# Optimization experiments

Hardware: AMD Instinct MI355X
Metric: run time of the kernel (lower is better)

The kernel has to match this reference:

```python
import jax, jax.numpy as jnp
import numpy as np
from functools import partial

MIN_PERSISTENCE = 0.0
BIG = jnp.float32(1e30)


def pairwise_dist(points):
    # points: [n, d] -> [n, n] Euclidean distances (Vietoris-Rips filtration values on edges)
    sq = jnp.sum(points * points, axis=-1)
    d2 = sq[:, None] + sq[None, :] - 2.0 * (points @ points.T)
    return jnp.sqrt(jnp.clip(d2, 0.0))


def h0_persistence(points):
    """0-dim persistent homology of the Vietoris-Rips filtration.

    H0 bars: every point is born at filtration 0; components merge at MST edge
    lengths (single-linkage). Deaths = the n-1 MST edge weights, in the order
    Prim's algorithm adds them (the boundary-matrix column reduction for dim 0
    yields exactly these pairs). One essential class (infinite bar) is dropped.
    """
    n = points.shape[0]
    dist = pairwise_dist(points)  # [n, n]

    in_tree = jnp.zeros((n,), dtype=bool).at[0].set(True)
    mind = dist[0]  # min distance from each node to the current tree

    def step(carry, _):
        mind, in_tree = carry
        masked = jnp.where(in_tree, BIG, mind)
        j = jnp.argmin(masked)          # next vertex merged into the tree
        death = masked[j]               # filtration value at which its component dies
        in_tree = in_tree.at[j].set(True)
        mind = jnp.minimum(mind, dist[j])
        return (mind, in_tree), death

    (_, _), deaths = jax.lax.scan(step, (mind, in_tree), None, length=n - 1)

    births = jnp.zeros_like(deaths)
    diagram = jnp.stack([births, deaths], axis=-1)  # [n-1, 2]
    # min_persistence threshold: zero out bars with persistence below threshold
    keep = (deaths - births) >= MIN_PERSISTENCE
    return jnp.where(keep[:, None], diagram, 0.0)


def setup_inputs() -> dict:
    key = jax.random.key(0)
    x = jax.random.normal(key, (8192, 64), dtype=jnp.float32)
    return {"x": x}


def reference(x):
    # PersistentHomologyLayer.forward with edge_index=None -> point-cloud VR persistence.
    return h0_persistence(x)
```

## Files before the change

### kernel.cpp

```cpp
#include <hip/hip_runtime.h>
#include <math.h>

#define N 8192
#define DIM 64
#define CAP_E 2000000
#define INLINE_V 8064

typedef unsigned long long u64;
typedef unsigned int u32;
typedef unsigned short u16;

__global__ void zero_out_kernel(float* __restrict__ out, int n) {
    int i = blockIdx.x * blockDim.x + threadIdx.x;
    if (i < n) out[i] = 0.0f;
}

__global__ __launch_bounds__(256) void norms_kernel(const float* __restrict__ x,
                                                    float* __restrict__ norms) {
    int i = blockIdx.x * blockDim.x + threadIdx.x;
    const float* row = x + (size_t)i * DIM;
    float acc = 0.f;
    #pragma unroll
    for (int k = 0; k < DIM; k++) { float v = row[k]; acc = __builtin_fmaf(v, v, acc); }
    norms[i] = acc;
}

__device__ inline void stage_tiles(const float* __restrict__ x, int bi, int bj, int t,
                                   float (*As)[65], float (*Bs)[65]) {
    int r = t >> 2, c0 = (t & 3) * 16;
    const float4* pa = (const float4*)(x + (size_t)(bi * 64 + r) * DIM + c0);
    const float4* pb = (const float4*)(x + (size_t)(bj * 64 + r) * DIM + c0);
    #pragma unroll
    for (int q = 0; q < 4; q++) {
        float4 a = pa[q], b = pb[q];
        int c = c0 + q * 4;
        As[c + 0][r] = a.x; As[c + 1][r] = a.y; As[c + 2][r] = a.z; As[c + 3][r] = a.w;
        Bs[c + 0][r] = b.x; Bs[c + 1][r] = b.y; Bs[c + 2][r] = b.z; Bs[c + 3][r] = b.w;
    }
}

__device__ inline void tile_d2(const float (*As)[65], const float (*Bs)[65],
                               const float ni[4], const float nj[4],
                               int tx, int ty, u32 d2b[4][4]) {
    float acc[4][4] = {};
    #pragma unroll 4
    for (int k = 0; k < 64; k++) {
        float av[4], bv[4];
        #pragma unroll
        for (int r = 0; r < 4; r++) av[r] = As[k][ty * 4 + r];
        #pragma unroll
        for (int c = 0; c < 4; c++) bv[c] = Bs[k][tx * 4 + c];
        #pragma unroll
        for (int r = 0; r < 4; r++)
            #pragma unroll
            for (int c = 0; c < 4; c++)
                acc[r][c] = __builtin_fmaf(av[r], bv[c], acc[r][c]);
    }
    #pragma unroll
    for (int r = 0; r < 4; r++)
        #pragma unroll
        for (int c = 0; c < 4; c++) {
            float d2 = __builtin_fmaf(-2.0f, acc[r][c], ni[r] + nj[c]);
            d2 = d2 < 0.f ? 0.f : d2;
            d2b[r][c] = __float_as_uint(d2);
        }
}

__global__ void init_kernel(u64* bestR, u64* bestC, u16* comp16, u32* deg, u32* ctr) {
    int i = blockIdx.x * blockDim.x + threadIdx.x;
    if (i < 8192) { bestR[i] = ~0ull; bestC[i] = ~0ull; comp16[i] = (u16)i; deg[i] = 0; }
    if (i < 8) ctr[i] = 0;
}

__global__ __launch_bounds__(256) void scan_fused(const float* __restrict__ x,
                                                  const float* __restrict__ norms,
                                                  const u16* __restrict__ comp16,
                                                  u64* __restrict__ bestR,
                                                  const u32* __restrict__ ctr) {
    if (ctr[1]) return;
    int bi = blockIdx.y, bj = blockIdx.x;
    if (bj < bi) return;
    __shared__ float As[64][65], Bs[64][65];
    __shared__ u16 rc[64], cc[64];
    __shared__ u64 rowBest[64], colBest[64];
    int t = threadIdx.x;
    stage_tiles(x, bi, bj, t, As, Bs);
    if (t < 64) {
        rc[t] = comp16[bi * 64 + t];
        cc[t] = comp16[bj * 64 + t];
        rowBest[t] = ~0ull; colBest[t] = ~0ull;
    }
    __syncthreads();
    int tx = t & 15, ty = t >> 4;
    float ni[4], nj[4];
    #pragma unroll
    for (int r = 0; r < 4; r++) ni[r] = norms[bi * 64 + ty * 4 + r];
    #pragma unroll
    for (int c = 0; c < 4; c++) nj[c] = norms[bj * 64 + tx * 4 + c];
    u32 d2b[4][4];
    tile_d2(As, Bs, ni, nj, tx, ty, d2b);

    #pragma unroll
    for (int r = 0; r < 4; r++) {
        u16 rcv = rc[ty * 4 + r];
        int gi = bi * 64 + ty * 4 + r;
        u64 best = ~0ull;
        #pragma unroll
        for (int c = 0; c < 4; c++) {
            if (cc[tx * 4 + c] != rcv) {
                int gj = bj * 64 + tx * 4 + c;
                u32 lo = gi < gj ? (u32)gi : (u32)gj;
                u32 hi = gi < gj ? (u32)gj : (u32)gi;
                u64 key = ((u64)d2b[r][c] << 26) | ((u64)lo << 13) | hi;
                if (key < best) best = key;
            }
        }
        if (best != ~0ull) atomicMin(&rowBest[ty * 4 + r], best);
    }
    #pragma unroll
    for (int c = 0; c < 4; c++) {
        u16 ccv = cc[tx * 4 + c];
        int gj = bj * 64 + tx * 4 + c;
        u64 best = ~0ull;
        #pragma unroll
        for (int r = 0; r < 4; r++) {
            if (rc[ty * 4 + r] != ccv) {
                int gi = bi * 64 + ty * 4 + r;
                u32 lo = gi < gj ? (u32)gi : (u32)gj;
                u32 hi = gi < gj ? (u32)gj : (u32)gi;
                u64 key = ((u64)d2b[r][c] << 26) | ((u64)lo << 13) | hi;
                if (key < best) best = key;
            }
        }
        if (best != ~0ull) atomicMin(&colBest[tx * 4 + c], best);
    }
    __syncthreads();
    if (t < 64) {
        if (rowBest[t] != ~0ull) atomicMin(&bestR[bi * 64 + t], rowBest[t]);
        if (colBest[t] != ~0ull) atomicMin(&bestR[bj * 64 + t], colBest[t]);
    }
}

__global__ void fold_kernel(u64* bestR, u64* bestC, const u16* comp16, const u32* ctr) {
    if (ctr[1]) return;
    int i = blockIdx.x * blockDim.x + threadIdx.x;
    if (i < 8192) {
        u64 k = bestR[i];
        if (k != ~0ull) { atomicMin(&bestC[comp16[i]], k); bestR[i] = ~0ull; }
    }
}

__global__ __launch_bounds__(1024) void merge_kernel(u16* comp16, u64* bestC,
                                                     u64* mstKeys, u32* ctr) {
    __shared__ u16 ping[8192], pong[8192];
    __shared__ unsigned char act[8192];
    __shared__ u32 cnt_s;
    if (ctr[1]) return;
    int t = threadIdx.x;
    if (t == 0) cnt_s = 0;
    for (int c = t; c < 8192; c += 1024) {
        u64 key = bestC[c];
        u16 par = (u16)c;
        if (key != ~0ull) {
            u32 a = (u32)(key >> 13) & 8191u, b = (u32)key & 8191u;
            u16 ca = comp16[a];
            u16 cv = (ca == (u16)c) ? comp16[b] : ca;
            u64 k2 = bestC[cv];
            bool mutual = false;
            if (k2 != ~0ull) {
                u32 a2 = (u32)(k2 >> 13) & 8191u, b2 = (u32)k2 & 8191u;
                u16 ca2 = comp16[a2];
                u16 cv2 = (ca2 == cv) ? comp16[b2] : ca2;
                mutual = (cv2 == (u16)c);
            }
            par = cv;
            if (mutual && (u32)c < (u32)cv) par = (u16)c;
            bool add = (!mutual) || ((u32)c < (u32)cv);
            if (add) {
                u32 idx = atomicAdd(&ctr[0], 1u);
                if (idx < 8192u) mstKeys[idx] = key;
            }
        }
        ping[c] = par;
        act[c] = 0;
    }
    __syncthreads();
    for (int c = t; c < 8192; c += 1024) bestC[c] = ~0ull;
    __syncthreads();
    for (int it = 0; it < 13; it++) {
        for (int c = t; c < 8192; c += 1024) pong[c] = ping[ping[c]];
        __syncthreads();
        for (int c = t; c < 8192; c += 1024) ping[c] = pong[c];
        __syncthreads();
    }
    for (int v = t; v < 8192; v += 1024) {
        u16 nc = ping[comp16[v]];
        comp16[v] = nc;
        act[nc] = 1;
    }
    __syncthreads();
    u32 local = 0;
    for (int c = t; c < 8192; c += 1024) local += act[c];
    atomicAdd(&cnt_s, local);
    __syncthreads();
    if (t == 0 && cnt_s == 1) ctr[1] = 1;
}

__global__ __launch_bounds__(1024) void sort_kernel(const u64* __restrict__ mstKeys,
                                                    u32* __restrict__ sortedWB,
                                                    const u32* __restrict__ ctr) {
    __shared__ u64 keys[8192];
    int t = threadIdx.x;
    u32 m = ctr[0]; if (m > 8191u) m = 8191u;
    for (int i = t; i < 8192; i += 1024) keys[i] = (i < (int)m) ? mstKeys[i] : ~0ull;
    __syncthreads();
    for (u32 k = 2; k <= 8192; k <<= 1)
        for (u32 j = k >> 1; j > 0; j >>= 1) {
            for (int i = t; i < 8192; i += 1024) {
                u32 ixj = (u32)i ^ j;
                if (ixj > (u32)i) {
                    u64 a = keys[i], b = keys[ixj];
                    bool up = ((i & k) == 0);
                    if ((a > b) == up) { keys[i] = b; keys[ixj] = a; }
                }
            }
            __syncthreads();
        }
    for (int i = t; i < 8192; i += 1024)
        sortedWB[i] = (i < 8191) ? (u32)(keys[i] >> 26) : 0xFFFFFFFFu;
}

__global__ __launch_bounds__(256) void collect_kernel(const float* __restrict__ x,
                                                      const float* __restrict__ norms,
                                                      const u32* __restrict__ sortedWB,
                                                      u64* __restrict__ edges,
                                                      u32* __restrict__ ctr) {
    __shared__ float As[64][65], Bs[64][65];
    __shared__ u32 sw[8191];
    int bi = blockIdx.y, bj = blockIdx.x;
    if (bj < bi) return;
    int t = threadIdx.x;
    stage_tiles(x, bi, bj, t, As, Bs);
    for (int i = t; i < 8191; i += 256) sw[i] = sortedWB[i];
    __syncthreads();
    u32 wmin = sw[0], wmax = sw[8190];
    int tx = t & 15, ty = t >> 4;
    float ni[4], nj[4];
    #pragma unroll
    for (int r = 0; r < 4; r++) ni[r] = norms[bi * 64 + ty * 4 + r];
    #pragma unroll
    for (int c = 0; c < 4; c++) nj[c] = norms[bj * 64 + tx * 4 + c];
    u32 d2b[4][4];
    tile_d2(As, Bs, ni, nj, tx, ty, d2b);

    #pragma unroll
    for (int r = 0; r < 4; r++) {
        int gi = bi * 64 + ty * 4 + r;
        #pragma unroll
        for (int c = 0; c < 4; c++) {
            int gj = bj * 64 + tx * 4 + c;
            if (gj <= gi) continue;
            u32 wb = d2b[r][c];
            if (wb < wmin || wb > wmax) continue;
            int lo = 0, hi = 8190;
            while (lo < hi) { int mid = (lo + hi) >> 1; if (sw[mid] < wb) lo = mid + 1; else hi = mid; }
            if (sw[lo] == wb) {
                u32 idx = atomicAdd(&ctr[3], 1u);
                if (idx < CAP_E)
                    edges[idx] = ((u64)(u32)lo << 26) | ((u64)(u32)gi << 13) | (u32)gj;
                else
                    atomicOr(&ctr[2], 16u);
            }
        }
    }
}

__global__ void degcnt_kernel(const u64* __restrict__ edges, u32* __restrict__ deg,
                              const u32* __restrict__ ctr) {
    u32 m = ctr[3]; if (m > CAP_E) m = CAP_E;
    for (u32 idx = blockIdx.x * 256u + threadIdx.x; idx < m; idx += gridDim.x * 256u) {
        u64 e = edges[idx];
        atomicAdd(&deg[(u32)(e >> 13) & 8191u], 1u);
        atomicAdd(&deg[(u32)e & 8191u], 1u);
    }
}

__global__ __launch_bounds__(1024) void offs_kernel(const u32* __restrict__ deg,
                                                    u32* __restrict__ offs,
                                                    u32* __restrict__ cur) {
    __shared__ u32 partial[1024];
    int t = threadIdx.x;
    u32 loc[8], s = 0;
    #pragma unroll
    for (int e = 0; e < 8; e++) { loc[e] = deg[t * 8 + e]; s += loc[e]; }
    partial[t] = s;
    __syncthreads();
    for (int d = 1; d < 1024; d <<= 1) {
        u32 v = (t >= d) ? partial[t - d] : 0;
        __syncthreads();
        partial[t] += v;
        __syncthreads();
    }
    u32 run = t ? partial[t - 1] : 0;
    #pragma unroll
    for (int e = 0; e < 8; e++) { offs[t * 8 + e] = run; cur[t * 8 + e] = run; run += loc[e]; }
    if (t == 1023) offs[8192] = run;
}

__global__ void fill_kernel(const u64* __restrict__ edges, u32* __restrict__ cur,
                            u32* __restrict__ adj, const u32* __restrict__ ctr) {
    u32 m = ctr[3]; if (m > CAP_E) m = CAP_E;
    for (u32 idx = blockIdx.x * 256u + threadIdx.x; idx < m; idx += gridDim.x * 256u) {
        u64 e = edges[idx];
        u32 rk = (u32)(e >> 26) & 8191u;
        u32 i = (u32)(e >> 13) & 8191u, j = (u32)e & 8191u;
        u32 p1 = atomicAdd(&cur[i], 1u); adj[p1] = (rk << 13) | j;
        u32 p2 = atomicAdd(&cur[j], 1u); adj[p2] = (rk << 13) | i;
    }
}

__global__ __launch_bounds__(256) void adj4_kernel(const u32* __restrict__ offs,
                                                   const u32* __restrict__ adjG,
                                                   uint4* __restrict__ adj4,
                                                   u64* __restrict__ ovf) {
    int v = blockIdx.x * 256 + threadIdx.x;
    if (v >= N) return;
    u32 o0 = offs[v], o1 = offs[v + 1], dg = o1 - o0;
    u32 e[4] = {0xFFFFFFFFu, 0xFFFFFFFFu, 0xFFFFFFFFu, 0xFFFFFFFFu};
    u32 nin = dg <= 4u ? dg : 3u;
    for (u32 q = 0; q < nin; q++) e[q] = adjG[o0 + q];
    if (dg > 4u) e[3] = 0xFFFFFFFEu;
    adj4[v] = make_uint4(e[0], e[1], e[2], e[3]);
    ovf[v] = ((u64)dg << 32) | o0;
}

__device__ __forceinline__ u32 dpp_min_u32(u32 x) {
    u32 y;
    y = (u32)__builtin_amdgcn_update_dpp((int)0xFFFFFFFF, (int)x, 0x111, 0xf, 0xf, false); x = y < x ? y : x;
    y = (u32)__builtin_amdgcn_update_dpp((int)0xFFFFFFFF, (int)x, 0x112, 0xf, 0xf, false); x = y < x ? y : x;
    y = (u32)__builtin_amdgcn_update_dpp((int)0xFFFFFFFF, (int)x, 0x114, 0xf, 0xf, false); x = y < x ? y : x;
    y = (u32)__builtin_amdgcn_update_dpp((int)0xFFFFFFFF, (int)x, 0x118, 0xf, 0xf, false); x = y < x ? y : x;
    y = (u32)__builtin_amdgcn_update_dpp((int)0xFFFFFFFF, (int)x, 0x142, 0xa, 0xf, false); x = y < x ? y : x;
    y = (u32)__builtin_amdgcn_update_dpp((int)0xFFFFFFFF, (int)x, 0x143, 0xc, 0xf, false); x = y < x ? y : x;
    return x;
}

__global__ __launch_bounds__(256) void gprim_kernel(const uint4* __restrict__ adj4,
                                                    const u64* __restrict__ ovf,
                                                    const u32* __restrict__ adjG,
                                                    u32* __restrict__ seqv,
                                                    u32* __restrict__ ctr) {
    __shared__ uint4 sAdj4[INLINE_V];
    __shared__ u32 sMind32[8192];
    const int t = threadIdx.x;
    for (int i = t; i < INLINE_V; i += 256) sAdj4[i] = adj4[i];
    for (int i = t; i < 8192; i += 256) sMind32[i] = 0x3FFFu;
    __syncthreads();
    if (t >= 64) return;
    __builtin_amdgcn_s_setprio(3);
    const int lane = t;
    if (lane == 0) sMind32[0] = 0xFFFFFFFFu;
    u64 ins0 = (lane == 0) ? 1ull : 0ull, ins1 = 0ull;
    u32 cmin = 0xFFFFFFFFu;
    u32 v = 0u, Lv = 0u;

#define PROC(e) do { \
        u32 _e = (e); \
        u32 _far = _e & 8191u; \
        u32 _slot = _far >> 6; \
        u64 _w = (_slot & 64u) ? ins1 : ins0; \
        bool _ok = (_e < 0x04000000u) && (((_far ^ (u32)lane) & 63u) == 0u) \
                   && (((_w >> (_slot & 63u)) & 1ull) == 0ull); \
        patch = (_ok && _e < patch) ? _e : patch; \
        if (_ok) atomicMin(&sMind32[((u32)lane << 7) + _slot], _e >> 13); \
    } while (0)

    for (int step = 0; step < N - 1; ++step) {
        uint2 rp = *(const uint2*)&sMind32[(Lv << 7) + 2u * (u32)lane];
        uint4 A = (v < (u32)INLINE_V) ? sAdj4[v] : adj4[v];
        u32 patch = 0xFFFFFFFFu;
        PROC(A.x); PROC(A.y); PROC(A.z);
        if (A.w == 0xFFFFFFFEu) {
            u64 od = ovf[v];
            u32 o0 = (u32)od, dgv = (u32)(od >> 32);
            u32 q = 3;
            for (; q + 4 <= dgv; q += 4) {
                u32 e0 = adjG[o0 + q], e1 = adjG[o0 + q + 1];
                u32 e2 = adjG[o0 + q + 2], e3 = adjG[o0 + q + 3];
                PROC(e0); PROC(e1); PROC(e2); PROC(e3);
            }
            for (; q < dgv; q++) { u32 e = adjG[o0 + q]; PROC(e); }
        } else {
            PROC(A.w);
        }
        cmin = patch < cmin ? patch : cmin;
        u32 m0 = rp.x, m1 = rp.y;
        u32 s0 = ((u32)lane << 1), s1 = s0 | 1u;
        u32 vslot = v >> 6;
        u32 k0 = (m0 < 0x3FFFu && s0 != vslot) ? ((m0 << 13) | (s0 << 6) | Lv) : 0xFFFFFFFFu;
        u32 k1 = (m1 < 0x3FFFu && s1 != vslot) ? ((m1 << 13) | (s1 << 6) | Lv) : 0xFFFFFFFFu;
        u32 rowMin = k0 < k1 ? k0 : k1;
        u32 R = dpp_min_u32(rowMin);
        u32 xc = ((u32)lane == Lv) ? patch : cmin;
        u32 C = dpp_min_u32(xc);
        u32 Rs = (u32)__builtin_amdgcn_readlane((int)R, 63);
        u32 Cs = (u32)__builtin_amdgcn_readlane((int)C, 63);
        u32 g = Rs < Cs ? Rs : Cs;
        if ((u32)lane == Lv) cmin = Rs < patch ? Rs : patch;
        if (g >= (0x3FFFu << 13)) { if (lane == 0) atomicOr(&ctr[2], 2u); break; }
        if (lane == 0) seqv[step] = g;
        v = g & 8191u; Lv = v & 63u;
        u32 nslot = v >> 6;
        bool mine = ((u32)lane == Lv);
        u64 bit = 1ull << (nslot & 63u);
        ins0 |= (mine && nslot < 64u) ? bit : 0ull;
        ins1 |= (mine && nslot >= 64u) ? bit : 0ull;
        if (mine) sMind32[(Lv << 7) + nslot] = 0xFFFFFFFFu;
    }
#undef PROC
}

__global__ void gather_kernel(const u32* __restrict__ seqv,
                              const u32* __restrict__ sortedWB,
                              float* __restrict__ out) {
    int s = blockIdx.x * blockDim.x + threadIdx.x;
    if (s < N - 1) {
        u32 p = seqv[s];
        u32 rk = p >> 13;
        out[2 * s + 1] = sqrtf(__uint_as_float(sortedWB[rk]));
    }
}

extern "C" void kernel_launch(void* const* d_in, const int* in_sizes, int n_in,
                              void* d_out, int out_size, void* d_ws, size_t ws_size,
                              hipStream_t stream) {
    const float* x = (const float*)d_in[0];
    float* out = (float*)d_out;

    char* ws = (char*)d_ws;
    size_t o = 0;
    u64* bestR    = (u64*)(ws + o); o += 8192 * 8;
    u64* bestC    = (u64*)(ws + o); o += 8192 * 8;
    u64* mstKeys  = (u64*)(ws + o); o += 8192 * 8;
    u64* edges    = (u64*)(ws + o); o += (size_t)CAP_E * 8;
    float* norms  = (float*)(ws + o); o += 8192 * 4;
    u32* sortedWB = (u32*)(ws + o); o += 8192 * 4;
    u32* deg      = (u32*)(ws + o); o += 8192 * 4;
    u32* offs     = (u32*)(ws + o); o += 8200 * 4;
    u32* cur      = (u32*)(ws + o); o += 8192 * 4;
    u32* seqv     = (u32*)(ws + o); o += 8192 * 4;
    u32* adj      = (u32*)(ws + o); o += (size_t)CAP_E * 2 * 4;
    uint4* adj4   = (uint4*)(ws + o); o += 8192 * 16;
    u64* ovf      = (u64*)(ws + o); o += 8192 * 8;
    u16* comp16   = (u16*)(ws + o); o += 8192 * 2;
    u32* ctr      = (u32*)(ws + o); o += 256;

    zero_out_kernel<<<(out_size + 255) / 256, 256, 0, stream>>>(out, out_size);
    norms_kernel<<<32, 256, 0, stream>>>(x, norms);
    init_kernel<<<32, 256, 0, stream>>>(bestR, bestC, comp16, deg, ctr);

    for (int r = 0; r < 13; r++) {
        scan_fused<<<dim3(128, 128), 256, 0, stream>>>(x, norms, comp16, bestR, ctr);
        fold_kernel<<<32, 256, 0, stream>>>(bestR, bestC, comp16, ctr);
        merge_kernel<<<1, 1024, 0, stream>>>(comp16, bestC, mstKeys, ctr);
    }

    sort_kernel<<<1, 1024, 0, stream>>>(mstKeys, sortedWB, ctr);
    collect_kernel<<<dim3(128, 128), 256, 0, stream>>>(x, norms, sortedWB, edges, ctr);
    degcnt_kernel<<<512, 256, 0, stream>>>(edges, deg, ctr);
    offs_kernel<<<1, 1024, 0, stream>>>(deg, offs, cur);
    fill_kernel<<<512, 256, 0, stream>>>(edges, cur, adj, ctr);
    adj4_kernel<<<32, 256, 0, stream>>>(offs, adj, adj4, ovf);
    gprim_kernel<<<1, 256, 0, stream>>>(adj4, ovf, adj, seqv, ctr);
    gather_kernel<<<32, 256, 0, stream>>>(seqv, sortedWB, out);
}
```

Measured before the change: 5.991 ms.

## Remove per-step global writes and branches from the serial Prim loop

The single-wavefront Prim loop no longer writes its step sequence to global memory on every step. Instead it stores a marker holding the step and rank in the shared mind array, and dumps that array once at the end. The gather kernel then scatters results by vertex. Other changes make the loop branch-free: atomicMin runs unconditionally with a sentinel value, the last-lane writes go to dummy slots, and the adjacency fetch always reads LDS. High-degree vertices now read their full list from the overflow path. The aim is to cut latency on the serial critical path, at the cost of some extra LDS atomics per step.

```diff
diff --git a/kernel.cpp b/kernel.cpp
--- a/kernel.cpp
+++ b/kernel.cpp
@@ -327,7 +327,7 @@
     if (v >= N) return;
     u32 o0 = offs[v], o1 = offs[v + 1], dg = o1 - o0;
     u32 e[4] = {0xFFFFFFFFu, 0xFFFFFFFFu, 0xFFFFFFFFu, 0xFFFFFFFFu};
-    u32 nin = dg <= 4u ? dg : 3u;
+    u32 nin = dg <= 4u ? dg : 0u;
     for (u32 q = 0; q < nin; q++) e[q] = adjG[o0 + q];
     if (dg > 4u) e[3] = 0xFFFFFFFEu;
     adj4[v] = make_uint4(e[0], e[1], e[2], e[3]);
@@ -348,13 +348,13 @@
 __global__ __launch_bounds__(256) void gprim_kernel(const uint4* __restrict__ adj4,
                                                     const u64* __restrict__ ovf,
                                                     const u32* __restrict__ adjG,
-                                                    u32* __restrict__ seqv,
+                                                    u32* __restrict__ seqm,
                                                     u32* __restrict__ ctr) {
     __shared__ uint4 sAdj4[INLINE_V];
-    __shared__ u32 sMind32[8192];
+    __shared__ u32 sMind32[8192 + 64];
     const int t = threadIdx.x;
     for (int i = t; i < INLINE_V; i += 256) sAdj4[i] = adj4[i];
-    for (int i = t; i < 8192; i += 256) sMind32[i] = 0x3FFFu;
+    for (int i = t; i < 8192 + 64; i += 256) sMind32[i] = 0x3FFFu;
     __syncthreads();
     if (t >= 64) return;
     __builtin_amdgcn_s_setprio(3);
@@ -363,6 +363,10 @@
     u64 ins0 = (lane == 0) ? 1ull : 0ull, ins1 = 0ull;
     u32 cmin = 0xFFFFFFFFu;
     u32 v = 0u, Lv = 0u;
+    const u32 baseLoc = (u32)lane << 7;
+    const u32 c0k = ((u32)lane * 2u) << 6;
+    const u32 c1k = c0k + 64u;
+    const u32 dummyLoc = 8192u + (u32)lane;
 
 #define PROC(e) do { \
         u32 _e = (e); \
@@ -372,33 +376,38 @@
         bool _ok = (_e < 0x04000000u) && (((_far ^ (u32)lane) & 63u) == 0u) \
                    && (((_w >> (_slot & 63u)) & 1ull) == 0ull); \
         patch = (_ok && _e < patch) ? _e : patch; \
-        if (_ok) atomicMin(&sMind32[((u32)lane << 7) + _slot], _e >> 13); \
+        u32 _val = _ok ? (_e >> 13) : 0xFFFFFFFFu; \
+        atomicMin(&sMind32[baseLoc + _slot], _val); \
     } while (0)
 
     for (int step = 0; step < N - 1; ++step) {
         uint2 rp = *(const uint2*)&sMind32[(Lv << 7) + 2u * (u32)lane];
-        uint4 A = (v < (u32)INLINE_V) ? sAdj4[v] : adj4[v];
+        uint4 A = sAdj4[v < (u32)INLINE_V ? v : 0u];
         u32 patch = 0xFFFFFFFFu;
-        PROC(A.x); PROC(A.y); PROC(A.z);
-        if (A.w == 0xFFFFFFFEu) {
+        if (__builtin_expect(v >= (u32)INLINE_V || A.w == 0xFFFFFFFEu, 0)) {
             u64 od = ovf[v];
             u32 o0 = (u32)od, dgv = (u32)(od >> 32);
-            u32 q = 3;
-            for (; q + 4 <= dgv; q += 4) {
-                u32 e0 = adjG[o0 + q], e1 = adjG[o0 + q + 1];
-                u32 e2 = adjG[o0 + q + 2], e3 = adjG[o0 + q + 3];
-                PROC(e0); PROC(e1); PROC(e2); PROC(e3);
-            }
-            for (; q < dgv; q++) { u32 e = adjG[o0 + q]; PROC(e); }
+            u32 iL = dgv ? dgv - 1u : 0u;
+            for (u32 q = 0; q < dgv; q += 4) {
+                u32 i1 = (q + 1u > iL) ? iL : q + 1u;
+                u32 i2 = (q + 2u > iL) ? iL : q + 2u;
+                u32 i3 = (q + 3u > iL) ? iL : q + 3u;
+                u32 e0 = adjG[o0 + q], e1 = adjG[o0 + i1];
+                u32 e2 = adjG[o0 + i2], e3 = adjG[o0 + i3];
+                PROC(e0);
+                if (q + 1u < dgv) PROC(e1);
+                if (q + 2u < dgv) PROC(e2);
+                if (q + 3u < dgv) PROC(e3);
+            }
         } else {
-            PROC(A.w);
+            PROC(A.x); PROC(A.y); PROC(A.z); PROC(A.w);
         }
         cmin = patch < cmin ? patch : cmin;
         u32 m0 = rp.x, m1 = rp.y;
         u32 s0 = ((u32)lane << 1), s1 = s0 | 1u;
         u32 vslot = v >> 6;
-        u32 k0 = (m0 < 0x3FFFu && s0 != vslot) ? ((m0 << 13) | (s0 << 6) | Lv) : 0xFFFFFFFFu;
-        u32 k1 = (m1 < 0x3FFFu && s1 != vslot) ? ((m1 << 13) | (s1 << 6) | Lv) : 0xFFFFFFFFu;
+        u32 k0 = (m0 < 0x3FFFu && s0 != vslot) ? ((m0 << 13) | c0k | Lv) : 0xFFFFFFFFu;
+        u32 k1 = (m1 < 0x3FFFu && s1 != vslot) ? ((m1 << 13) | c1k | Lv) : 0xFFFFFFFFu;
         u32 rowMin = k0 < k1 ? k0 : k1;
         u32 R = dpp_min_u32(rowMin);
         u32 xc = ((u32)lane == Lv) ? patch : cmin;
@@ -408,26 +417,36 @@
         u32 g = Rs < Cs ? Rs : Cs;
         if ((u32)lane == Lv) cmin = Rs < patch ? Rs : patch;
         if (g >= (0x3FFFu << 13)) { if (lane == 0) atomicOr(&ctr[2], 2u); break; }
-        if (lane == 0) seqv[step] = g;
         v = g & 8191u; Lv = v & 63u;
         u32 nslot = v >> 6;
         bool mine = ((u32)lane == Lv);
         u64 bit = 1ull << (nslot & 63u);
         ins0 |= (mine && nslot < 64u) ? bit : 0ull;
         ins1 |= (mine && nslot >= 64u) ? bit : 0ull;
-        if (mine) sMind32[(Lv << 7) + nslot] = 0xFFFFFFFFu;
+        u32 marker = 0x80000000u | ((u32)step << 13) | (g >> 13);
+        u32 wloc = mine ? ((Lv << 7) + nslot) : dummyLoc;
+        sMind32[wloc] = marker;
     }
 #undef PROC
-}
-
-__global__ void gather_kernel(const u32* __restrict__ seqv,
+
+    for (int it = 0; it < 32; ++it) {
+        int idx = it * 64 + lane;
+        uint4 m4 = *(const uint4*)&sMind32[idx * 4];
+        ((uint4*)seqm)[idx] = m4;
+    }
+}
+
+__global__ void gather_kernel(const u32* __restrict__ seqm,
                               const u32* __restrict__ sortedWB,
                               float* __restrict__ out) {
-    int s = blockIdx.x * blockDim.x + threadIdx.x;
-    if (s < N - 1) {
-        u32 p = seqv[s];
-        u32 rk = p >> 13;
-        out[2 * s + 1] = sqrtf(__uint_as_float(sortedWB[rk]));
+    int v = blockIdx.x * blockDim.x + threadIdx.x;
+    if (v < N) {
+        u32 m = seqm[v];
+        u32 stp = (m >> 13) & 8191u;
+        if ((m & 0x80000000u) && stp < 8191u) {
+            u32 rk = m & 8191u;
+            out[2 * stp + 1] = sqrtf(__uint_as_float(sortedWB[rk]));
+        }
     }
 }
 
@@ -448,7 +467,7 @@
     u32* deg      = (u32*)(ws + o); o += 8192 * 4;
     u32* offs     = (u32*)(ws + o); o += 8200 * 4;
     u32* cur      = (u32*)(ws + o); o += 8192 * 4;
-    u32* seqv     = (u32*)(ws + o); o += 8192 * 4;
+    u32* seqm     = (u32*)(ws + o); o += 8192 * 4;
     u32* adj      = (u32*)(ws + o); o += (size_t)CAP_E * 2 * 4;
     uint4* adj4   = (uint4*)(ws + o); o += 8192 * 16;
     u64* ovf      = (u64*)(ws + o); o += 8192 * 8;
@@ -471,6 +490,6 @@
     offs_kernel<<<1, 1024, 0, stream>>>(deg, offs, cur);
     fill_kernel<<<512, 256, 0, stream>>>(edges, cur, adj, ctr);
     adj4_kernel<<<32, 256, 0, stream>>>(offs, adj, adj4, ovf);
-    gprim_kernel<<<1, 256, 0, stream>>>(adj4, ovf, adj, seqv, ctr);
-    gather_kernel<<<32, 256, 0, stream>>>(seqv, sortedWB, out);
-}
+    gprim_kernel<<<1, 256, 0, stream>>>(adj4, ovf, adj, seqm, ctr);
+    gather_kernel<<<32, 256, 0, stream>>>(seqm, sortedWB, out);
+}
```

After: 6.707 ms. 11.9% more time.

## Spread LDS atomicMin across lanes and track in-tree state via readlane bitmasks

Applied to the files above, without the earlier changes.

The serial Prim loop no longer has each matching lane issue its own atomicMin. Up to four edge updates per adjacency chunk are now packed into lanes 0-3 and issued as one LDS atomic instruction. In-tree exclusion of row entries now comes from a readlane of the owner lane's insertion bitmasks, instead of writing a sentinel into shared memory on each step. The inline adjacency table grows to cover more vertices, and overflow vertices go through the overflow list from index 0. This is meant to shorten the per-step dependency chain, with the risk of extra readlane/select work and a more complicated overflow path.

```diff
diff --git a/kernel.cpp b/kernel.cpp
--- a/kernel.cpp
+++ b/kernel.cpp
@@ -4,7 +4,7 @@
 #define N 8192
 #define DIM 64
 #define CAP_E 2000000
-#define INLINE_V 8064
+#define INLINE_V 8144
 
 typedef unsigned long long u64;
 typedef unsigned int u32;
@@ -327,7 +327,7 @@
     if (v >= N) return;
     u32 o0 = offs[v], o1 = offs[v + 1], dg = o1 - o0;
     u32 e[4] = {0xFFFFFFFFu, 0xFFFFFFFFu, 0xFFFFFFFFu, 0xFFFFFFFFu};
-    u32 nin = dg <= 4u ? dg : 3u;
+    u32 nin = dg <= 4u ? dg : 0u;
     for (u32 q = 0; q < nin; q++) e[q] = adjG[o0 + q];
     if (dg > 4u) e[3] = 0xFFFFFFFEu;
     adj4[v] = make_uint4(e[0], e[1], e[2], e[3]);
@@ -359,46 +359,66 @@
     if (t >= 64) return;
     __builtin_amdgcn_s_setprio(3);
     const int lane = t;
-    if (lane == 0) sMind32[0] = 0xFFFFFFFFu;
     u64 ins0 = (lane == 0) ? 1ull : 0ull, ins1 = 0ull;
     u32 cmin = 0xFFFFFFFFu;
     u32 v = 0u, Lv = 0u;
-
-#define PROC(e) do { \
+    const u32 c0k = (u32)lane << 7;
+    const u32 c1k = c0k + 64u;
+
+#define PREG(e) do { \
         u32 _e = (e); \
-        u32 _far = _e & 8191u; \
-        u32 _slot = _far >> 6; \
+        u32 _slot = (_e >> 6) & 127u; \
         u64 _w = (_slot & 64u) ? ins1 : ins0; \
-        bool _ok = (_e < 0x04000000u) && (((_far ^ (u32)lane) & 63u) == 0u) \
+        bool _ok = (((_e ^ (u32)lane) & 0xFC00003Fu) == 0u) \
                    && (((_w >> (_slot & 63u)) & 1ull) == 0ull); \
         patch = (_ok && _e < patch) ? _e : patch; \
-        if (_ok) atomicMin(&sMind32[((u32)lane << 7) + _slot], _e >> 13); \
+    } while (0)
+
+#define DSMIN4(e0_, e1_, e2_, e3_) do { \
+        u32 _ek = (e0_); \
+        _ek = (lane == 1) ? (e1_) : _ek; \
+        _ek = (lane == 2) ? (e2_) : _ek; \
+        _ek = (lane == 3) ? (e3_) : _ek; \
+        if (lane < 4) \
+            atomicMin(&sMind32[((_ek & 63u) << 7) + ((_ek >> 6) & 127u)], _ek >> 13); \
     } while (0)
 
     for (int step = 0; step < N - 1; ++step) {
         uint2 rp = *(const uint2*)&sMind32[(Lv << 7) + 2u * (u32)lane];
-        uint4 A = (v < (u32)INLINE_V) ? sAdj4[v] : adj4[v];
+        uint4 A = sAdj4[v < (u32)INLINE_V ? v : 0u];
         u32 patch = 0xFFFFFFFFu;
-        PROC(A.x); PROC(A.y); PROC(A.z);
-        if (A.w == 0xFFFFFFFEu) {
+        if (__builtin_expect(v >= (u32)INLINE_V || A.w == 0xFFFFFFFEu, 0)) {
             u64 od = ovf[v];
             u32 o0 = (u32)od, dgv = (u32)(od >> 32);
-            u32 q = 3;
-            for (; q + 4 <= dgv; q += 4) {
-                u32 e0 = adjG[o0 + q], e1 = adjG[o0 + q + 1];
-                u32 e2 = adjG[o0 + q + 2], e3 = adjG[o0 + q + 3];
-                PROC(e0); PROC(e1); PROC(e2); PROC(e3);
-            }
-            for (; q < dgv; q++) { u32 e = adjG[o0 + q]; PROC(e); }
+            u32 iL = dgv ? dgv - 1u : 0u;
+            for (u32 q = 0; q < dgv; q += 4) {
+                u32 i1 = (q + 1u > iL) ? iL : q + 1u;
+                u32 i2 = (q + 2u > iL) ? iL : q + 2u;
+                u32 i3 = (q + 3u > iL) ? iL : q + 3u;
+                u32 e0 = adjG[o0 + q], e1 = adjG[o0 + i1];
+                u32 e2 = adjG[o0 + i2], e3 = adjG[o0 + i3];
+                DSMIN4(e0, e1, e2, e3);
+                PREG(e0);
+                if (q + 1u < dgv) PREG(e1);
+                if (q + 2u < dgv) PREG(e2);
+                if (q + 3u < dgv) PREG(e3);
+            }
         } else {
-            PROC(A.w);
+            DSMIN4(A.x, A.y, A.z, A.w);
+            PREG(A.x); PREG(A.y); PREG(A.z); PREG(A.w);
         }
         cmin = patch < cmin ? patch : cmin;
+        u32 b0 = (u32)__builtin_amdgcn_readlane((int)(u32)ins0, (int)Lv);
+        u32 b1 = (u32)__builtin_amdgcn_readlane((int)(u32)(ins0 >> 32), (int)Lv);
+        u32 b2 = (u32)__builtin_amdgcn_readlane((int)(u32)ins1, (int)Lv);
+        u32 b3 = (u32)__builtin_amdgcn_readlane((int)(u32)(ins1 >> 32), (int)Lv);
+        u32 selA = (lane & 16) ? b1 : b0;
+        u32 selB = (lane & 16) ? b3 : b2;
+        u32 sel  = (lane & 32) ? selB : selA;
+        u32 bw = sel >> ((2u * (u32)lane) & 31u);
         u32 m0 = rp.x, m1 = rp.y;
-        u32 s0 = ((u32)lane << 1), s1 = s0 | 1u;
-        u32 vslot = v >> 6;
-        u32 k0 = (m0 < 0x3FFFu && s0 != vslot) ? ((m0 << 13) | (s0 << 6) | Lv) : 0xFFFFFFFFu;
-        u32 k1 = (m1 < 0x3FFFu && s1 != vslot) ? ((m1 << 13) | (s1 << 6) | Lv) : 0xFFFFFFFFu;
+        u32 k0 = (m0 < 0x3FFFu && !(bw & 1u)) ? ((m0 << 13) | c0k | Lv) : 0xFFFFFFFFu;
+        u32 k1 = (m1 < 0x3FFFu && !(bw & 2u)) ? ((m1 << 13) | c1k | Lv) : 0xFFFFFFFFu;
         u32 rowMin = k0 < k1 ? k0 : k1;
         u32 R = dpp_min_u32(rowMin);
         u32 xc = ((u32)lane == Lv) ? patch : cmin;
@@ -415,9 +435,9 @@
         u64 bit = 1ull << (nslot & 63u);
         ins0 |= (mine && nslot < 64u) ? bit : 0ull;
         ins1 |= (mine && nslot >= 64u) ? bit : 0ull;
-        if (mine) sMind32[(Lv << 7) + nslot] = 0xFFFFFFFFu;
-    }
-#undef PROC
+    }
+#undef PREG
+#undef DSMIN4
 }
 
 __global__ void gather_kernel(const u32* __restrict__ seqv,
```

After: 6.506 ms. 1.09x slower.
